# Optimization experiments

Hardware: AMD Instinct MI355X
Metric: run time of the kernel (lower is better)

The kernel has to match this reference:

```python
import jax, jax.numpy as jnp
import numpy as np

DIM = 16        # lagrangian.dim -> y has 2*DIM phase-space coords
HID = 128       # hidden width of the parametric Lagrangian
BATCH = 32768


def setup_inputs() -> dict:
    key = jax.random.key(0)
    k1, k2, k3, k4 = jax.random.split(key, 4)
    y = jax.random.normal(k1, (BATCH, 2 * DIM), dtype=jnp.float32)
    # small-scale init keeps J_{qdot,qdot} = I + (MLP Hessian block) well conditioned
    W1 = jax.random.normal(k2, (HID, 2 * DIM), dtype=jnp.float32) * (1.0 / np.sqrt(2 * DIM))
    b1 = jax.random.normal(k3, (HID,), dtype=jnp.float32) * 0.1
    w2 = jax.random.normal(k4, (HID,), dtype=jnp.float32) * 0.1
    return {"y": y, "W1": W1, "b1": b1, "w2": w2}


def _lagrangian(y_vec, W1, b1, w2):
    """Scalar Lagrangian L(q, qdot) for a single phase-space vector y_vec [2*DIM]."""
    qdot = y_vec[DIM:]
    kinetic = 0.5 * jnp.dot(qdot, qdot)
    return kinetic + jnp.dot(w2, jnp.tanh(W1 @ y_vec + b1))


def reference(y, W1, b1, w2):
    """Acceleration qdotdot = (dL/dq - qdot . J_{q,qdot}) . J_{qdot,qdot}^{-1}.

    Instead of the original O(dim^2) repeated tf.gradients calls, compute the
    full gradient and Hessian once per sample via fused forward-over-reverse
    autodiff, vmapped over the batch.
    """
    d = DIM
    L = lambda yv: _lagrangian(yv, W1, b1, w2)
    grad_fn = jax.grad(L)
    hess_fn = jax.jacfwd(grad_fn)  # forward-over-reverse Hessian, one sweep

    g = jax.vmap(grad_fn)(y)   # [B, 2d]   full dL/dy
    H = jax.vmap(hess_fn)(y)   # [B, 2d, 2d]  full Hessian d2L/(dy dy)

    qdot = y[:, d:]            # [B, d]
    dLdq = g[:, :d]            # [B, d]
    J_qqdot = H[:, :d, d:]     # [B, d, d]  d2L/(dq_i dqdot_j)
    J_qdqd_inv = jnp.linalg.inv(H[:, d:, d:])  # [B, d, d]

    rhs = dLdq - jnp.einsum('bi,bij->bj', qdot, J_qqdot)
    qdotdot = jnp.einsum('bi,bij->bj', rhs, J_qdqd_inv)
    return qdotdot
```

## Files before the change

kernel.cpp:

```cpp
#include <hip/hip_runtime.h>
#include <math.h>

#define DIMQ 16
#define HID  128
#define SPB  64
#define NTHREADS 512

typedef __attribute__((ext_vector_type(8))) _Float16 f16x8;
typedef __attribute__((ext_vector_type(4))) _Float16 f16x4;
typedef __attribute__((ext_vector_type(4))) float f32x4;
typedef __attribute__((ext_vector_type(2))) float v2f;

#define OFF_WFF  0
#define OFF_ABT  8192
#define OFF_USP  16384
#define OFF_SST  49152
#define OFF_MSCR 0
#define LDS_BYTES 81920

__device__ __forceinline__ int axor(int row, int off) { return off ^ ((row & 7) << 3); }
__device__ __forceinline__ int mswz(int s, int off) {
    return s * 320 + (off ^ ((s & 7) << 2));
}
__device__ __forceinline__ f16x8 pack8(float4 a, float4 b) {
    f16x8 r;
    r[0]=(_Float16)a.x; r[1]=(_Float16)a.y; r[2]=(_Float16)a.z; r[3]=(_Float16)a.w;
    r[4]=(_Float16)b.x; r[5]=(_Float16)b.y; r[6]=(_Float16)b.z; r[7]=(_Float16)b.w;
    return r;
}

__global__ __launch_bounds__(NTHREADS, 4)
void lag_accel_kernel(const float* __restrict__ y,
                      const float* __restrict__ W1,
                      const float* __restrict__ b1,
                      const float* __restrict__ w2,
                      float* __restrict__ out)
{
    __shared__ __align__(16) char smem[LDS_BYTES];
    _Float16* Wff = (_Float16*)(smem + OFF_WFF);
    _Float16* ABT = (_Float16*)(smem + OFF_ABT);
    _Float16* usp = (_Float16*)(smem + OFF_USP);
    _Float16* sst = (_Float16*)(smem + OFF_SST);

    const int tid = threadIdx.x;
    const long long s0 = (long long)blockIdx.x * SPB;

    const int wave = tid >> 6;
    const int lane = tid & 63;
    const int grp  = lane >> 4;
    const int j    = lane & 15;
    const int ht   = wave;

    f16x8 yf[4];
#pragma unroll
    for (int st = 0; st < 4; ++st) {
        const float4* yg = (const float4*)(y + (s0 + st * 16 + j) * 32 + (grp << 3));
        yf[st] = pack8(yg[0], yg[1]);
    }

    {
        const int ht_ = tid >> 6, grp_ = (tid >> 4) & 3, j_ = tid & 15;
        const float4* src = (const float4*)(W1 + (ht_ * 16 + j_) * 32 + (grp_ << 3));
        *(f16x8*)&Wff[tid * 8] = pack8(src[0], src[1]);
    }
    {
        const int k = tid & 31, h0 = (tid >> 5) << 3;
        float v[8];
#pragma unroll
        for (int i = 0; i < 8; ++i) v[i] = W1[(h0 + i) * 32 + k];
        f16x8 p;
#pragma unroll
        for (int i = 0; i < 8; ++i) p[i] = (_Float16)v[i];
        const int j_ = (k < 16) ? k : (k - 16);
        const int off = (k < 16) ? h0 : (128 + h0);
        *(f16x8*)&ABT[(j_ << 8) + axor(j_, off)] = p;
    }

    __syncthreads();

    f16x8 aW  = *(const f16x8*)&Wff[((ht * 4 + grp) * 16 + j) * 8];
    f16x8 aAl = *(const f16x8*)&Wff[((ht * 4 + (grp & 1)) * 16 + j) * 8];
    f16x8 aA;
#pragma unroll
    for (int e = 0; e < 8; ++e) aA[e] = (grp >= 2) ? aAl[e] : (_Float16)0.0f;
    float4 b1v = *(const float4*)&b1[ht * 16 + (grp << 2)];
    float4 w2v = *(const float4*)&w2[ht * 16 + (grp << 2)];
    f32x4 ci; ci[0] = b1v.x; ci[1] = b1v.y; ci[2] = b1v.z; ci[3] = b1v.w;
    const f32x4 zf = {0.0f, 0.0f, 0.0f, 0.0f};
    const int h4 = ht * 16 + (grp << 2);

#pragma unroll
    for (int st = 0; st < 4; ++st) {
        f32x4 zacc = __builtin_amdgcn_mfma_f32_16x16x32_f16(aW, yf[st], ci, 0, 0, 0);
        f32x4 aacc = __builtin_amdgcn_mfma_f32_16x16x32_f16(aA, yf[st], zf, 0, 0, 0);
        const int smp2 = st * 16 + j;
        _Float16 su[4], sn[4], sv[4];
#pragma unroll
        for (int r = 0; r < 4; ++r) {
            float z  = zacc[r], aq = aacc[r];
            float w2c = (r == 0) ? w2v.x : (r == 1) ? w2v.y
                       : (r == 2) ? w2v.z : w2v.w;
            float e  = __expf(2.0f * z);
            float rr = 2.0f * __builtin_amdgcn_rcpf(e + 1.0f);
            float t_ = 1.0f - rr;
            float u  = w2c * (rr * (2.0f - rr));
            float s  = -2.0f * t_ * u;
            float sp = s * aq;
            su[r] = (_Float16)u; sn[r] = (_Float16)(-sp);
            sv[r] = (_Float16)s;
        }
        f16x4 pa = {su[0], su[1], su[2], su[3]};
        f16x4 pb = {sn[0], sn[1], sn[2], sn[3]};
        f16x4 pc = {sv[0], sv[1], sv[2], sv[3]};
        *(f16x4*)&usp[(smp2 << 8) + axor(smp2, h4)]       = pa;
        *(f16x4*)&usp[(smp2 << 8) + axor(smp2, 128 + h4)] = pb;
        *(f16x4*)&sst[(smp2 << 7) + axor(smp2, h4)]       = pc;
    }

    __syncthreads();

    f32x4 racc = {0.0f, 0.0f, 0.0f, 0.0f};
    if (wave < 4) {
        const int smp = wave * 16 + j;
#pragma unroll
        for (int kc = 0; kc < 8; ++kc) {
            const int o = (kc << 5) + (grp << 3);
            f16x8 af = *(const f16x8*)&ABT[(j << 8) + axor(j, o)];
            f16x8 bf = *(const f16x8*)&usp[(smp << 8) + axor(smp, o)];
            racc = __builtin_amdgcn_mfma_f32_16x16x32_f16(af, bf, racc, 0, 0, 0);
        }
    }

    f32x4 acc[8];
    {
        f32x4 ident;
#pragma unroll
        for (int r = 0; r < 4; ++r) ident[r] = ((grp << 2) + r == j) ? 1.0f : 0.0f;
#pragma unroll
        for (int gs = 0; gs < 8; ++gs) acc[gs] = ident;
    }
#pragma unroll
    for (int kc = 0; kc < 4; ++kc) {
        const int o = (kc << 5) + (grp << 3);
        f16x8 bfrag = *(const f16x8*)&ABT[(j << 8) + axor(j, 128 + o)];
#pragma unroll
        for (int gs = 0; gs < 8; ++gs) {
            const int smp = wave * 8 + gs;
            f16x8 sfrag = *(const f16x8*)&sst[(smp << 7) + axor(smp, o)];
            f16x8 afrag = sfrag * bfrag;
            acc[gs] = __builtin_amdgcn_mfma_f32_16x16x32_f16(afrag, bfrag, acc[gs], 0, 0, 0);
        }
    }

    __syncthreads();

    float* Mscr = (float*)(smem + OFF_MSCR);
#pragma unroll
    for (int gs = 0; gs < 8; ++gs) {
        float4 v;
        v.x = acc[gs][0]; v.y = acc[gs][1]; v.z = acc[gs][2]; v.w = acc[gs][3];
        *(float4*)&Mscr[mswz(wave * 8 + gs, j * 20 + (grp << 2))] = v;
    }

    __syncthreads();

    if (wave >= 4) return;
    const int sl = lane & 15;
    const int rb = lane >> 4;
    const int s  = wave * 16 + sl;

    v2f M2[4][8];
    float r4[4], d4[4];
#pragma unroll
    for (int r = 0; r < 4; ++r) {
        const int ro = (4 * rb + r) * 20;
        float4 v0 = *(const float4*)&Mscr[mswz(s, ro + 0)];
        float4 v1 = *(const float4*)&Mscr[mswz(s, ro + 4)];
        float4 v2 = *(const float4*)&Mscr[mswz(s, ro + 8)];
        float4 v3 = *(const float4*)&Mscr[mswz(s, ro + 12)];
        M2[r][0] = (v2f){v0.x, v0.y}; M2[r][1] = (v2f){v0.z, v0.w};
        M2[r][2] = (v2f){v1.x, v1.y}; M2[r][3] = (v2f){v1.z, v1.w};
        M2[r][4] = (v2f){v2.x, v2.y}; M2[r][5] = (v2f){v2.z, v2.w};
        M2[r][6] = (v2f){v3.x, v3.y}; M2[r][7] = (v2f){v3.z, v3.w};
        r4[r] = racc[r];
        d4[r] = 1.0f;
    }

#pragma unroll
    for (int k = 0; k < 16; ++k) {
        const int src = sl + ((k >> 2) << 4);
        float piv = __shfl(M2[k & 3][k >> 1][k & 1], src, 64);
        float rk  = __shfl(r4[k & 3], src, 64);
        float invp = __builtin_amdgcn_rcpf(piv);
        invp = invp * (2.0f - piv * invp);
        float f[4];
#pragma unroll
        for (int r = 0; r < 4; ++r) {
            float fr = M2[r][k >> 1][k & 1] * invp;
            const bool isk = ((rb << 2) + r) == k;
            f[r]  = isk ? 0.0f : fr;
            d4[r] = isk ? piv : d4[r];
            r4[r] = fmaf(-f[r], rk, r4[r]);
        }
        const int i2s = (k >> 1) + (k & 1);
#pragma unroll
        for (int i2 = i2s; i2 < 8; ++i2) {
            float p0 = (2 * i2 == k) ? piv : __shfl(M2[k & 3][i2][0], src, 64);
            float p1 = __shfl(M2[k & 3][i2][1], src, 64);
            v2f pv = {p0, p1};
#pragma unroll
            for (int r = 0; r < 4; ++r) {
                v2f fv = {-f[r], -f[r]};
                M2[r][i2] = __builtin_elementwise_fma(fv, pv, M2[r][i2]);
            }
        }
    }

    float4 xo;
    {
        float i0 = __builtin_amdgcn_rcpf(d4[0]); i0 = i0 * (2.0f - d4[0] * i0);
        float i1 = __builtin_amdgcn_rcpf(d4[1]); i1 = i1 * (2.0f - d4[1] * i1);
        float i2 = __builtin_amdgcn_rcpf(d4[2]); i2 = i2 * (2.0f - d4[2] * i2);
        float i3 = __builtin_amdgcn_rcpf(d4[3]); i3 = i3 * (2.0f - d4[3] * i3);
        xo.x = r4[0] * i0; xo.y = r4[1] * i1; xo.z = r4[2] * i2; xo.w = r4[3] * i3;
    }
    *(float4*)&out[(s0 + s) * DIMQ + (rb << 2)] = xo;
}

extern "C" void kernel_launch(void* const* d_in, const int* in_sizes, int n_in,
                              void* d_out, int out_size, void* d_ws, size_t ws_size,
                              hipStream_t stream) {
    const float* y  = (const float*)d_in[0];
    const float* W1 = (const float*)d_in[1];
    const float* b1 = (const float*)d_in[2];
    const float* w2 = (const float*)d_in[3];
    float* out = (float*)d_out;
    const int batch = in_sizes[0] / 32;
    const int blocks = (batch + SPB - 1) / SPB;
    lag_accel_kernel<<<blocks, NTHREADS, 0, stream>>>(y, W1, b1, w2, out);
}
```

Baseline: 18.95 us.

## Spread Gauss-Jordan solve across all eight waves with two rows per lane

The per-sample 16x16 Gauss-Jordan solve previously ran on only four waves, with 16 lanes per sample and 4 rows per lane. It now runs on all eight waves, with 8 lanes per sample and 2 rows per lane. To do this the RHS vector from the MFMA accumulator is staged through LDS scratch (column 16 of each row) so any wave can read it. This halves the per-lane serial FMA chain and uses idle waves, at the cost of an extra LDS store and read, and scalar output stores instead of a float4 store.

```diff
diff --git a/kernel.cpp b/kernel.cpp
--- a/kernel.cpp
+++ b/kernel.cpp
@@ -161,70 +161,73 @@
         v.x = acc[gs][0]; v.y = acc[gs][1]; v.z = acc[gs][2]; v.w = acc[gs][3];
         *(float4*)&Mscr[mswz(wave * 8 + gs, j * 20 + (grp << 2))] = v;
     }
-
-    __syncthreads();
-
-    if (wave >= 4) return;
-    const int sl = lane & 15;
-    const int rb = lane >> 4;
-    const int s  = wave * 16 + sl;
-
-    v2f M2[4][8];
-    float r4[4], d4[4];
-#pragma unroll
-    for (int r = 0; r < 4; ++r) {
-        const int ro = (4 * rb + r) * 20;
+    if (wave < 4) {
+        const int smp = wave * 16 + j;
+#pragma unroll
+        for (int r = 0; r < 4; ++r)
+            Mscr[mswz(smp, ((grp << 2) + r) * 20 + 16)] = racc[r];
+    }
+
+    __syncthreads();
+
+    const int sl = lane >> 3;
+    const int rw = lane & 7;
+    const int s  = wave * 8 + sl;
+
+    v2f M2[2][8];
+    float r2[2], d2[2];
+#pragma unroll
+    for (int rr = 0; rr < 2; ++rr) {
+        const int row = rw + (rr << 3);
+        const int ro = row * 20;
         float4 v0 = *(const float4*)&Mscr[mswz(s, ro + 0)];
         float4 v1 = *(const float4*)&Mscr[mswz(s, ro + 4)];
         float4 v2 = *(const float4*)&Mscr[mswz(s, ro + 8)];
         float4 v3 = *(const float4*)&Mscr[mswz(s, ro + 12)];
-        M2[r][0] = (v2f){v0.x, v0.y}; M2[r][1] = (v2f){v0.z, v0.w};
-        M2[r][2] = (v2f){v1.x, v1.y}; M2[r][3] = (v2f){v1.z, v1.w};
-        M2[r][4] = (v2f){v2.x, v2.y}; M2[r][5] = (v2f){v2.z, v2.w};
-        M2[r][6] = (v2f){v3.x, v3.y}; M2[r][7] = (v2f){v3.z, v3.w};
-        r4[r] = racc[r];
-        d4[r] = 1.0f;
+        M2[rr][0] = (v2f){v0.x, v0.y}; M2[rr][1] = (v2f){v0.z, v0.w};
+        M2[rr][2] = (v2f){v1.x, v1.y}; M2[rr][3] = (v2f){v1.z, v1.w};
+        M2[rr][4] = (v2f){v2.x, v2.y}; M2[rr][5] = (v2f){v2.z, v2.w};
+        M2[rr][6] = (v2f){v3.x, v3.y}; M2[rr][7] = (v2f){v3.z, v3.w};
+        r2[rr] = Mscr[mswz(s, ro + 16)];
+        d2[rr] = 1.0f;
     }
 
 #pragma unroll
     for (int k = 0; k < 16; ++k) {
-        const int src = sl + ((k >> 2) << 4);
-        float piv = __shfl(M2[k & 3][k >> 1][k & 1], src, 64);
-        float rk  = __shfl(r4[k & 3], src, 64);
+        const int src = (lane & 56) | (k & 7);
+        const int kr = k >> 3;
+        float piv = __shfl(M2[kr][k >> 1][k & 1], src, 64);
+        float rk  = __shfl(r2[kr], src, 64);
         float invp = __builtin_amdgcn_rcpf(piv);
         invp = invp * (2.0f - piv * invp);
-        float f[4];
-#pragma unroll
-        for (int r = 0; r < 4; ++r) {
-            float fr = M2[r][k >> 1][k & 1] * invp;
-            const bool isk = ((rb << 2) + r) == k;
-            f[r]  = isk ? 0.0f : fr;
-            d4[r] = isk ? piv : d4[r];
-            r4[r] = fmaf(-f[r], rk, r4[r]);
-        }
+        float f0 = M2[0][k >> 1][k & 1] * invp;
+        float f1 = M2[1][k >> 1][k & 1] * invp;
+        const bool isk0 = (rw == k);
+        const bool isk1 = (rw + 8 == k);
+        f0 = isk0 ? 0.0f : f0;  d2[0] = isk0 ? piv : d2[0];
+        f1 = isk1 ? 0.0f : f1;  d2[1] = isk1 ? piv : d2[1];
+        r2[0] = fmaf(-f0, rk, r2[0]);
+        r2[1] = fmaf(-f1, rk, r2[1]);
         const int i2s = (k >> 1) + (k & 1);
 #pragma unroll
         for (int i2 = i2s; i2 < 8; ++i2) {
-            float p0 = (2 * i2 == k) ? piv : __shfl(M2[k & 3][i2][0], src, 64);
-            float p1 = __shfl(M2[k & 3][i2][1], src, 64);
+            float p0 = (2 * i2 == k) ? piv : __shfl(M2[kr][i2][0], src, 64);
+            float p1 = __shfl(M2[kr][i2][1], src, 64);
             v2f pv = {p0, p1};
-#pragma unroll
-            for (int r = 0; r < 4; ++r) {
-                v2f fv = {-f[r], -f[r]};
-                M2[r][i2] = __builtin_elementwise_fma(fv, pv, M2[r][i2]);
-            }
-        }
-    }
-
-    float4 xo;
-    {
-        float i0 = __builtin_amdgcn_rcpf(d4[0]); i0 = i0 * (2.0f - d4[0] * i0);
-        float i1 = __builtin_amdgcn_rcpf(d4[1]); i1 = i1 * (2.0f - d4[1] * i1);
-        float i2 = __builtin_amdgcn_rcpf(d4[2]); i2 = i2 * (2.0f - d4[2] * i2);
-        float i3 = __builtin_amdgcn_rcpf(d4[3]); i3 = i3 * (2.0f - d4[3] * i3);
-        xo.x = r4[0] * i0; xo.y = r4[1] * i1; xo.z = r4[2] * i2; xo.w = r4[3] * i3;
-    }
-    *(float4*)&out[(s0 + s) * DIMQ + (rb << 2)] = xo;
+            v2f fv0 = {-f0, -f0};
+            v2f fv1 = {-f1, -f1};
+            M2[0][i2] = __builtin_elementwise_fma(fv0, pv, M2[0][i2]);
+            M2[1][i2] = __builtin_elementwise_fma(fv1, pv, M2[1][i2]);
+        }
+    }
+
+    {
+        float i0 = __builtin_amdgcn_rcpf(d2[0]); i0 = i0 * (2.0f - d2[0] * i0);
+        float i1 = __builtin_amdgcn_rcpf(d2[1]); i1 = i1 * (2.0f - d2[1] * i1);
+        float* ob = out + (s0 + s) * DIMQ;
+        ob[rw]     = r2[0] * i0;
+        ob[rw + 8] = r2[1] * i1;
+    }
 }
 
 extern "C" void kernel_launch(void* const* d_in, const int* in_sizes, int n_in,
```

After: 22.02 us. 16.2% more time.
